# Optimization experiments

Hardware: AMD Instinct MI355X
Metric: run time of the kernel (lower is better)

The kernel has to match this reference:

```python
import jax, jax.numpy as jnp
import numpy as np

N, NFEAT, NHID1, NHID2 = 16384, 128, 128, 64

def setup_inputs() -> dict:
    key = jax.random.key(0)
    k1, k2, k3, k4 = jax.random.split(key, 4)
    feature = jax.random.normal(k1, (N, NFEAT), dtype=jnp.float32)
    # dense (row-normalized) adjacency surrogate
    adj = jax.random.uniform(k2, (N, N), dtype=jnp.float32) / N
    W1 = jax.random.normal(k3, (NFEAT, NHID1), dtype=jnp.float32) / np.sqrt(NFEAT)
    b1 = jnp.zeros((NHID1,), dtype=jnp.float32)
    W2 = jax.random.normal(k4, (NHID1, NHID2), dtype=jnp.float32) / np.sqrt(NHID1)
    b2 = jnp.zeros((NHID2,), dtype=jnp.float32)
    return {"feature": feature, "adj": adj, "W1": W1, "b1": b1, "W2": W2, "b2": b2}

def reference(feature, adj, W1, b1, W2, b2):
    # layer 1: support = X@W1; agg = A@support; relu
    h = jax.nn.relu(adj @ (feature @ W1) + b1)
    # dropout is identity in eval mode
    # layer 2
    out = adj @ (h @ W2) + b2
    return out
```

## Files before the change

### kernel.cpp

```cpp
#include <hip/hip_runtime.h>
#include <stdint.h>

typedef float  f32x4  __attribute__((ext_vector_type(4)));
typedef short  short8 __attribute__((ext_vector_type(8)));
typedef __bf16 bf16x8 __attribute__((ext_vector_type(8)));

__device__ __forceinline__ unsigned short f2bf(float f) {
    unsigned u = __builtin_bit_cast(unsigned, f);
    unsigned r = u + 0x7fffu + ((u >> 16) & 1u);
    return (unsigned short)(r >> 16);
}

__device__ __forceinline__ short8 cvt8(f32x4 a, f32x4 b) {
    short8 r;
    r[0] = (short)f2bf(a[0]); r[1] = (short)f2bf(a[1]);
    r[2] = (short)f2bf(a[2]); r[3] = (short)f2bf(a[3]);
    r[4] = (short)f2bf(b[0]); r[5] = (short)f2bf(b[1]);
    r[6] = (short)f2bf(b[2]); r[7] = (short)f2bf(b[3]);
    return r;
}

typedef const __attribute__((address_space(1))) void* gas_p;
typedef __attribute__((address_space(3))) void*       las_p;
__device__ __forceinline__ void gld_lds16(const void* g, void* l) {
    __builtin_amdgcn_global_load_lds((gas_p)g, (las_p)l, 16, 0, 0);
}

__device__ __forceinline__ f32x4 mfma16(short8 a, short8 b, f32x4 c) {
    return __builtin_amdgcn_mfma_f32_16x16x32_bf16(
        __builtin_bit_cast(bf16x8, a), __builtin_bit_cast(bf16x8, b), c, 0, 0, 0);
}

template<int NMAT>
__global__ __launch_bounds__(256) void k_xw_t(const float* __restrict__ X,
                                              const float* __restrict__ W,
                                              short* __restrict__ St, int M) {
    constexpr int K   = 128;
    constexpr int NPT = NMAT / 4;
    __shared__ float Xs[64][129];
    __shared__ float Ws[K][NMAT];

    const int tid = threadIdx.x;
    const int m0  = blockIdx.x * 64;

    constexpr int WCH = K * NMAT / 4 / 256;
    #pragma unroll
    for (int j = 0; j < WCH; ++j) {
        int ch = tid + j * 256;
        ((float4*)Ws)[ch] = ((const float4*)W)[ch];
    }
    #pragma unroll
    for (int j = 0; j < 8; ++j) {
        int ch = tid + j * 256;
        int r = ch >> 5, c4 = ch & 31;
        float4 v = *(const float4*)(X + (size_t)(m0 + r) * K + c4 * 4);
        Xs[r][c4 * 4 + 0] = v.x; Xs[r][c4 * 4 + 1] = v.y;
        Xs[r][c4 * 4 + 2] = v.z; Xs[r][c4 * 4 + 3] = v.w;
    }
    __syncthreads();

    const int m  = tid & 63;
    const int n0 = (tid >> 6) * NPT;
    float acc[NPT];
    #pragma unroll
    for (int i = 0; i < NPT; ++i) acc[i] = 0.f;

    for (int k = 0; k < K; ++k) {
        float x = Xs[m][k];
        #pragma unroll
        for (int i = 0; i < NPT; i += 4) {
            float4 w = *(const float4*)&Ws[k][n0 + i];
            acc[i + 0] += x * w.x; acc[i + 1] += x * w.y;
            acc[i + 2] += x * w.z; acc[i + 3] += x * w.w;
        }
    }
    #pragma unroll
    for (int i = 0; i < NPT; ++i)
        St[(size_t)(n0 + i) * M + m0 + m] = (short)f2bf(acc[i]);
}

template<int BN, bool RELU>
__global__ __launch_bounds__(256, 1) void k_adj_gemm(const float* __restrict__ A,
                                                     const short* __restrict__ Bt,
                                                     const float* __restrict__ bias,
                                                     float* __restrict__ out,
                                                     int M, int K) {
    constexpr int BM   = 64, BK = 64;
    constexpr int NF   = BN / 16;
    constexpr int BCH  = BN * BK * 2 / (256 * 16);
    constexpr int VMH  = BCH + 16;
    constexpr int VML  = BCH;

    __shared__ short Bs[4][BN * 64];

    const int tid  = threadIdx.x;
    const int wave = tid >> 6, lane = tid & 63;
    const int lr   = lane & 15, lk = lane >> 4;
    const int row0 = blockIdx.x * BM;
    const int row_g = row0 + wave * 16 + lr;

    const char* Abase = (const char*)A + (size_t)row_g * K * 4 + lk * 32;

    const int key   = (lr & 7) << 4;
    const int offs0 = (lk * 16) ^ key;
    const int offs1 = (64 + lk * 16) ^ key;

    f32x4 acc[NF];
    #pragma unroll
    for (int n = 0; n < NF; ++n) acc[n] = (f32x4)0.f;

    f32x4 bA0[16], bA1[16];
    const int NT  = K / BK;
    const int NTM = NT - 1;

#define LOAD_SLOT(QARR, BI, TT)                                                 \
    {                                                                           \
        const char* p = Abase + (size_t)(TT) * 256;                             \
        QARR[(BI) + 0] = *(const f32x4*)(p);                                    \
        QARR[(BI) + 1] = *(const f32x4*)(p + 16);                               \
        QARR[(BI) + 2] = *(const f32x4*)(p + 128);                              \
        QARR[(BI) + 3] = *(const f32x4*)(p + 144);                              \
    }
#define LOAD_BATCH(QARR, T0)                                                    \
    {                                                                           \
        LOAD_SLOT(QARR, 0,  ((T0) + 0) & NTM)                                   \
        LOAD_SLOT(QARR, 4,  ((T0) + 1) & NTM)                                   \
        LOAD_SLOT(QARR, 8,  ((T0) + 2) & NTM)                                   \
        LOAD_SLOT(QARR, 12, ((T0) + 3) & NTM)                                   \
    }
#define STAGE_B(BUF, KTP)                                                       \
    {                                                                           \
        _Pragma("unroll")                                                       \
        for (int j = 0; j < BCH; ++j) {                                         \
            int o = (tid + j * 256) * 16;          \
            int r = o >> 7, w = o & 127;                                        \
            const char* src = (const char*)Bt + (size_t)r * (K * 2)             \
                              + (size_t)(KTP) * 128 + (w ^ ((r & 7) << 4));     \
            gld_lds16(src, (char*)&Bs[BUF][0] + o);                             \
        }                                                                       \
    }

    LOAD_BATCH(bA0, 0)
    STAGE_B(0, 0)
    LOAD_BATCH(bA1, 4)

#define ITER(KT, QARR, J4, CB, NB, VM, BATCH_STMT)                              \
    {                                                                           \
                        \
        short8 fa0 = cvt8(QARR[(J4) + 0], QARR[(J4) + 1]);                      \
        short8 fa1 = cvt8(QARR[(J4) + 2], QARR[(J4) + 3]);                      \
        { int ktn = ((KT) + 1) & NTM; STAGE_B(NB, ktn) }                        \
        BATCH_STMT                                                              \
        __builtin_amdgcn_sched_barrier(0);                                      \
            \
        asm volatile("s_waitcnt vmcnt(%0)" :: "i"(VM) : "memory");              \
        __builtin_amdgcn_s_barrier();                     \
        __builtin_amdgcn_sched_barrier(0);                                      \
        _Pragma("unroll")                                                       \
        for (int n = 0; n < NF; ++n) {                                          \
            short8 b0 = *(const short8*)((const char*)&Bs[CB][0]                \
                                         + n * 2048 + lr * 128 + offs0);        \
            acc[n] = mfma16(fa0, b0, acc[n]);                                   \
            short8 b1 = *(const short8*)((const char*)&Bs[CB][0]                \
                                         + n * 2048 + lr * 128 + offs1);        \
            acc[n] = mfma16(fa1, b1, acc[n]);                                   \
        }                                                                       \
    }

    for (int g = 0; g < 32; ++g) {
        int t = g * 8;
        ITER(t + 0, bA0, 0,  0, 1, VMH, )
        ITER(t + 1, bA0, 4,  1, 2, VML, )
        ITER(t + 2, bA0, 8,  2, 3, VML, )
        ITER(t + 3, bA0, 12, 3, 0, VMH, LOAD_BATCH(bA0, (t + 3) + 5))
        ITER(t + 4, bA1, 0,  0, 1, VMH, )
        ITER(t + 5, bA1, 4,  1, 2, VML, )
        ITER(t + 6, bA1, 8,  2, 3, VML, )
        ITER(t + 7, bA1, 12, 3, 0, VMH, LOAD_BATCH(bA1, (t + 7) + 5))
    }
#undef ITER
#undef LOAD_BATCH
#undef LOAD_SLOT
#undef STAGE_B

    #pragma unroll
    for (int n = 0; n < NF; ++n) {
        int col = n * 16 + lr;
        float bv = bias[col];
        #pragma unroll
        for (int j = 0; j < 4; ++j) {
            int row = row0 + wave * 16 + lk * 4 + j;
            float v = acc[n][j] + bv;
            if (RELU) v = fmaxf(v, 0.f);
            out[(size_t)row * BN + col] = v;
        }
    }
}

extern "C" void kernel_launch(void* const* d_in, const int* in_sizes, int n_in,
                              void* d_out, int out_size, void* d_ws, size_t ws_size,
                              hipStream_t stream) {
    const int N = 16384, NH1 = 128, NH2 = 64;
    const float* feature = (const float*)d_in[0];
    const float* adj     = (const float*)d_in[1];
    const float* W1      = (const float*)d_in[2];
    const float* b1      = (const float*)d_in[3];
    const float* W2      = (const float*)d_in[4];
    const float* b2      = (const float*)d_in[5];

    short* S1t = (short*)d_ws;
    float* h   = (float*)((char*)d_ws + (4u << 20));
    short* S2t = (short*)((char*)d_ws + (12u << 20));

    k_xw_t<NH1><<<N / 64, 256, 0, stream>>>(feature, W1, S1t, N);
    k_adj_gemm<NH1, true ><<<N / 64, 256, 0, stream>>>(adj, S1t, b1, h, N, N);
    k_xw_t<NH2><<<N / 64, 256, 0, stream>>>(h, W2, S2t, N);
    k_adj_gemm<NH2, false><<<N / 64, 256, 0, stream>>>(adj, S2t, b2, (float*)d_out, N, N);
    (void)in_sizes; (void)n_in; (void)out_size; (void)ws_size;
}
```

Measured before the change: 486.8 us.

## Stage B tiles in bursts of four with eight LDS buffers

Replaces the per-iteration single-tile B staging (4 LDS buffers) with a burst that stages four B tiles plus the next A register batch at once into an 8-buffer LDS ring, with graded vmcnt waits per iteration. The aim is to issue memory loads in larger groups and keep more tiles in flight, hiding global latency in the adjacency GEMM. It doubles LDS use for B and changes the wait accounting, which could reduce occupancy or introduce stalls if the vmcnt thresholds are off.

```diff
diff --git a/kernel.cpp b/kernel.cpp
--- a/kernel.cpp
+++ b/kernel.cpp
@@ -88,10 +88,12 @@
     constexpr int BM   = 64, BK = 64;
     constexpr int NF   = BN / 16;
     constexpr int BCH  = BN * BK * 2 / (256 * 16);
-    constexpr int VMH  = BCH + 16;
-    constexpr int VML  = BCH;
-
-    __shared__ short Bs[4][BN * 64];
+    constexpr int VM0  = 7 * BCH + 32;
+    constexpr int VM1  = 6 * BCH + 32;
+    constexpr int VM2  = 5 * BCH + 32;
+    constexpr int VM3  = 4 * BCH + 32;
+
+    __shared__ short Bs[8][BN * 64];
 
     const int tid  = threadIdx.x;
     const int wave = tid >> 6, lane = tid & 63;
@@ -128,31 +130,34 @@
         LOAD_SLOT(QARR, 8,  ((T0) + 2) & NTM)                                   \
         LOAD_SLOT(QARR, 12, ((T0) + 3) & NTM)                                   \
     }
-#define STAGE_B(BUF, KTP)                                                       \
+#define STAGE_B1(BUF, KTP)                                                      \
     {                                                                           \
         _Pragma("unroll")                                                       \
         for (int j = 0; j < BCH; ++j) {                                         \
             int o = (tid + j * 256) * 16;          \
             int r = o >> 7, w = o & 127;                                        \
             const char* src = (const char*)Bt + (size_t)r * (K * 2)             \
-                              + (size_t)(KTP) * 128 + (w ^ ((r & 7) << 4));     \
+                              + (size_t)((KTP) & NTM) * 128 + (w ^ ((r & 7) << 4)); \
             gld_lds16(src, (char*)&Bs[BUF][0] + o);                             \
         }                                                                       \
     }
-
-    LOAD_BATCH(bA0, 0)
-    STAGE_B(0, 0)
-    LOAD_BATCH(bA1, 4)
-
-#define ITER(KT, QARR, J4, CB, NB, VM, BATCH_STMT)                              \
-    {                                                                           \
-                        \
+#define STAGE_BURST(BF0, QARR, T0)                                              \
+    STAGE_B1((BF0) + 0, (T0) + 0)                                               \
+    STAGE_B1((BF0) + 1, (T0) + 1)                                               \
+    STAGE_B1((BF0) + 2, (T0) + 2)                                               \
+    STAGE_B1((BF0) + 3, (T0) + 3)                                               \
+    LOAD_BATCH(QARR, T0)
+
+    STAGE_BURST(0, bA1, 0)
+
+#define ITER(KT, QARR, J4, CB, VM, STAGE_STMT)                                  \
+    {                                                                           \
+                   \
         short8 fa0 = cvt8(QARR[(J4) + 0], QARR[(J4) + 1]);                      \
         short8 fa1 = cvt8(QARR[(J4) + 2], QARR[(J4) + 3]);                      \
-        { int ktn = ((KT) + 1) & NTM; STAGE_B(NB, ktn) }                        \
-        BATCH_STMT                                                              \
+        STAGE_STMT                                                              \
         __builtin_amdgcn_sched_barrier(0);                                      \
-            \
+                   \
         asm volatile("s_waitcnt vmcnt(%0)" :: "i"(VM) : "memory");              \
         __builtin_amdgcn_s_barrier();                     \
         __builtin_amdgcn_sched_barrier(0);                                      \
@@ -167,21 +172,22 @@
         }                                                                       \
     }
 
-    for (int g = 0; g < 32; ++g) {
-        int t = g * 8;
-        ITER(t + 0, bA0, 0,  0, 1, VMH, )
-        ITER(t + 1, bA0, 4,  1, 2, VML, )
-        ITER(t + 2, bA0, 8,  2, 3, VML, )
-        ITER(t + 3, bA0, 12, 3, 0, VMH, LOAD_BATCH(bA0, (t + 3) + 5))
-        ITER(t + 4, bA1, 0,  0, 1, VMH, )
-        ITER(t + 5, bA1, 4,  1, 2, VML, )
-        ITER(t + 6, bA1, 8,  2, 3, VML, )
-        ITER(t + 7, bA1, 12, 3, 0, VMH, LOAD_BATCH(bA1, (t + 7) + 5))
+    for (int d = 0; d < 32; ++d) {
+        int t = d * 8;
+        ITER(t + 0, bA1, 0,  0, VM0, STAGE_BURST(4, bA0, (t) + 4))
+        ITER(t + 1, bA1, 4,  1, VM1, )
+        ITER(t + 2, bA1, 8,  2, VM2, )
+        ITER(t + 3, bA1, 12, 3, VM3, )
+        ITER(t + 4, bA0, 0,  4, VM0, STAGE_BURST(0, bA1, (t) + 8))
+        ITER(t + 5, bA0, 4,  5, VM1, )
+        ITER(t + 6, bA0, 8,  6, VM2, )
+        ITER(t + 7, bA0, 12, 7, VM3, )
     }
 #undef ITER
+#undef STAGE_BURST
+#undef STAGE_B1
 #undef LOAD_BATCH
 #undef LOAD_SLOT
-#undef STAGE_B
 
     #pragma unroll
     for (int n = 0; n < NF; ++n) {
```

After: 489.7 us. About the same (+0.6%).

## Write bf16 adjacency during first aggregation and reuse it in second GEMM

Applied to the files above, without the earlier changes.

The first adjacency GEMM now also stores its bf16-converted A fragments to a 512 MB workspace buffer, laid out in fragment order. The second GEMM reads those pre-converted fragments instead of re-reading the fp32 adjacency, which halves its A traffic and removes its conversion work. The cost is 512 MB of extra writes in the first kernel plus more workspace, and the vmcnt waits are adjusted to account for the added stores.

```diff
diff --git a/kernel.cpp b/kernel.cpp
--- a/kernel.cpp
+++ b/kernel.cpp
@@ -79,17 +79,17 @@
         St[(size_t)(n0 + i) * M + m0 + m] = (short)f2bf(acc[i]);
 }
 
-template<int BN, bool RELU>
-__global__ __launch_bounds__(256, 1) void k_adj_gemm(const float* __restrict__ A,
-                                                     const short* __restrict__ Bt,
-                                                     const float* __restrict__ bias,
-                                                     float* __restrict__ out,
-                                                     int M, int K) {
-    constexpr int BM   = 64, BK = 64;
-    constexpr int NF   = BN / 16;
-    constexpr int BCH  = BN * BK * 2 / (256 * 16);
-    constexpr int VMH  = BCH + 16;
-    constexpr int VML  = BCH;
+__global__ __launch_bounds__(256, 1) void k_adj_cvt(const float* __restrict__ A,
+                                                    const short* __restrict__ Bt,
+                                                    const float* __restrict__ bias,
+                                                    float* __restrict__ out,
+                                                    char* __restrict__ adj16,
+                                                    int M, int K) {
+    constexpr int BM  = 64, BK = 64, BN = 128;
+    constexpr int NF  = BN / 16;
+    constexpr int BCH = BN * BK * 2 / (256 * 16);
+    constexpr int VMH = BCH + 18;
+    constexpr int VML = BCH + 2;
 
     __shared__ short Bs[4][BN * 64];
 
@@ -100,6 +100,7 @@
     const int row_g = row0 + wave * 16 + lr;
 
     const char* Abase = (const char*)A + (size_t)row_g * K * 4 + lk * 32;
+    char* Cbase = adj16 + (size_t)blockIdx.x * 256 * 8192 + tid * 32;
 
     const int key   = (lr & 7) << 4;
     const int offs0 = (lk * 16) ^ key;
@@ -132,10 +133,10 @@
     {                                                                           \
         _Pragma("unroll")                                                       \
         for (int j = 0; j < BCH; ++j) {                                         \
-            int o = (tid + j * 256) * 16;          \
+            int o = (tid + j * 256) * 16;                                       \
             int r = o >> 7, w = o & 127;                                        \
             const char* src = (const char*)Bt + (size_t)r * (K * 2)             \
-                              + (size_t)(KTP) * 128 + (w ^ ((r & 7) << 4));     \
+                              + (size_t)((KTP) & NTM) * 128 + (w ^ ((r & 7) << 4)); \
             gld_lds16(src, (char*)&Bs[BUF][0] + o);                             \
         }                                                                       \
     }
@@ -146,15 +147,13 @@
 
 #define ITER(KT, QARR, J4, CB, NB, VM, BATCH_STMT)                              \
     {                                                                           \
-                        \
         short8 fa0 = cvt8(QARR[(J4) + 0], QARR[(J4) + 1]);                      \
         short8 fa1 = cvt8(QARR[(J4) + 2], QARR[(J4) + 3]);                      \
         { int ktn = ((KT) + 1) & NTM; STAGE_B(NB, ktn) }                        \
         BATCH_STMT                                                              \
         __builtin_amdgcn_sched_barrier(0);                                      \
-            \
         asm volatile("s_waitcnt vmcnt(%0)" :: "i"(VM) : "memory");              \
-        __builtin_amdgcn_s_barrier();                     \
+        __builtin_amdgcn_s_barrier();                                           \
         __builtin_amdgcn_sched_barrier(0);                                      \
         _Pragma("unroll")                                                       \
         for (int n = 0; n < NF; ++n) {                                          \
@@ -165,6 +164,9 @@
                                          + n * 2048 + lr * 128 + offs1);        \
             acc[n] = mfma16(fa1, b1, acc[n]);                                   \
         }                                                                       \
+        __builtin_amdgcn_sched_barrier(0);                                      \
+        { char* dst = Cbase + (size_t)(KT) * 8192;                              \
+          *(short8*)(dst) = fa0; *(short8*)(dst + 16) = fa1; }                  \
     }
 
     for (int g = 0; g < 32; ++g) {
@@ -179,9 +181,9 @@
         ITER(t + 7, bA1, 12, 3, 0, VMH, LOAD_BATCH(bA1, (t + 7) + 5))
     }
 #undef ITER
+#undef STAGE_B
 #undef LOAD_BATCH
 #undef LOAD_SLOT
-#undef STAGE_B
 
     #pragma unroll
     for (int n = 0; n < NF; ++n) {
@@ -190,9 +192,117 @@
         #pragma unroll
         for (int j = 0; j < 4; ++j) {
             int row = row0 + wave * 16 + lk * 4 + j;
-            float v = acc[n][j] + bv;
-            if (RELU) v = fmaxf(v, 0.f);
-            out[(size_t)row * BN + col] = v;
+            out[(size_t)row * BN + col] = fmaxf(acc[n][j] + bv, 0.f);
+        }
+    }
+}
+
+__global__ __launch_bounds__(256, 1) void k_adj_pre(const char* __restrict__ adj16,
+                                                    const short* __restrict__ Bt,
+                                                    const float* __restrict__ bias,
+                                                    float* __restrict__ out,
+                                                    int M, int K) {
+    constexpr int BM  = 64, BK = 64, BN = 64;
+    constexpr int NF  = BN / 16;
+    constexpr int BCH = BN * BK * 2 / (256 * 16);
+    constexpr int VMH = BCH + 8;
+    constexpr int VML = BCH;
+
+    __shared__ short Bs[4][BN * 64];
+
+    const int tid  = threadIdx.x;
+    const int wave = tid >> 6, lane = tid & 63;
+    const int lr   = lane & 15, lk = lane >> 4;
+    const int row0 = blockIdx.x * BM;
+
+    const char* Cbase = adj16 + (size_t)blockIdx.x * 256 * 8192 + tid * 32;
+
+    const int key   = (lr & 7) << 4;
+    const int offs0 = (lk * 16) ^ key;
+    const int offs1 = (64 + lk * 16) ^ key;
+
+    f32x4 acc[NF];
+    #pragma unroll
+    for (int n = 0; n < NF; ++n) acc[n] = (f32x4)0.f;
+
+    uint4 bA0[8], bA1[8];
+    const int NT  = K / BK;
+    const int NTM = NT - 1;
+
+#define LOAD_SLOT(QARR, BI, TT)                                                 \
+    {                                                                           \
+        const char* p = Cbase + (size_t)(TT) * 8192;                            \
+        QARR[(BI) + 0] = *(const uint4*)(p);                                    \
+        QARR[(BI) + 1] = *(const uint4*)(p + 16);                               \
+    }
+#define LOAD_BATCH(QARR, T0)                                                    \
+    {                                                                           \
+        LOAD_SLOT(QARR, 0, ((T0) + 0) & NTM)                                    \
+        LOAD_SLOT(QARR, 2, ((T0) + 1) & NTM)                                    \
+        LOAD_SLOT(QARR, 4, ((T0) + 2) & NTM)                                    \
+        LOAD_SLOT(QARR, 6, ((T0) + 3) & NTM)                                    \
+    }
+#define STAGE_B(BUF, KTP)                                                       \
+    {                                                                           \
+        _Pragma("unroll")                                                       \
+        for (int j = 0; j < BCH; ++j) {                                         \
+            int o = (tid + j * 256) * 16;                                       \
+            int r = o >> 7, w = o & 127;                                        \
+            const char* src = (const char*)Bt + (size_t)r * (K * 2)             \
+                              + (size_t)((KTP) & NTM) * 128 + (w ^ ((r & 7) << 4)); \
+            gld_lds16(src, (char*)&Bs[BUF][0] + o);                             \
+        }                                                                       \
+    }
+
+    LOAD_BATCH(bA0, 0)
+    STAGE_B(0, 0)
+    LOAD_BATCH(bA1, 4)
+
+#define ITER(KT, QARR, J4, CB, NB, VM, BATCH_STMT)                              \
+    {                                                                           \
+        short8 fa0 = __builtin_bit_cast(short8, QARR[(J4) + 0]);                \
+        short8 fa1 = __builtin_bit_cast(short8, QARR[(J4) + 1]);                \
+        { int ktn = ((KT) + 1) & NTM; STAGE_B(NB, ktn) }                        \
+        BATCH_STMT                                                              \
+        __builtin_amdgcn_sched_barrier(0);                                      \
+        asm volatile("s_waitcnt vmcnt(%0)" :: "i"(VM) : "memory");              \
+        __builtin_amdgcn_s_barrier();                                           \
+        __builtin_amdgcn_sched_barrier(0);                                      \
+        _Pragma("unroll")                                                       \
+        for (int n = 0; n < NF; ++n) {                                          \
+            short8 b0 = *(const short8*)((const char*)&Bs[CB][0]                \
+                                         + n * 2048 + lr * 128 + offs0);        \
+            acc[n] = mfma16(fa0, b0, acc[n]);                                   \
+            short8 b1 = *(const short8*)((const char*)&Bs[CB][0]                \
+                                         + n * 2048 + lr * 128 + offs1);        \
+            acc[n] = mfma16(fa1, b1, acc[n]);                                   \
+        }                                                                       \
+    }
+
+    for (int g = 0; g < 32; ++g) {
+        int t = g * 8;
+        ITER(t + 0, bA0, 0, 0, 1, VMH, )
+        ITER(t + 1, bA0, 2, 1, 2, VML, )
+        ITER(t + 2, bA0, 4, 2, 3, VML, )
+        ITER(t + 3, bA0, 6, 3, 0, VMH, LOAD_BATCH(bA0, (t + 3) + 5))
+        ITER(t + 4, bA1, 0, 0, 1, VMH, )
+        ITER(t + 5, bA1, 2, 1, 2, VML, )
+        ITER(t + 6, bA1, 4, 2, 3, VML, )
+        ITER(t + 7, bA1, 6, 3, 0, VMH, LOAD_BATCH(bA1, (t + 7) + 5))
+    }
+#undef ITER
+#undef STAGE_B
+#undef LOAD_BATCH
+#undef LOAD_SLOT
+
+    #pragma unroll
+    for (int n = 0; n < NF; ++n) {
+        int col = n * 16 + lr;
+        float bv = bias[col];
+        #pragma unroll
+        for (int j = 0; j < 4; ++j) {
+            int row = row0 + wave * 16 + lk * 4 + j;
+            out[(size_t)row * BN + col] = acc[n][j] + bv;
         }
     }
 }
@@ -208,13 +318,14 @@
     const float* W2      = (const float*)d_in[4];
     const float* b2      = (const float*)d_in[5];
 
-    short* S1t = (short*)d_ws;
-    float* h   = (float*)((char*)d_ws + (4u << 20));
-    short* S2t = (short*)((char*)d_ws + (12u << 20));
+    short* S1t  = (short*)d_ws;
+    float* h    = (float*)((char*)d_ws + (4u << 20));
+    short* S2t  = (short*)((char*)d_ws + (12u << 20));
+    char*  a16  = (char*)d_ws + (16u << 20);
 
     k_xw_t<NH1><<<N / 64, 256, 0, stream>>>(feature, W1, S1t, N);
-    k_adj_gemm<NH1, true ><<<N / 64, 256, 0, stream>>>(adj, S1t, b1, h, N, N);
+    k_adj_cvt <<<N / 64, 256, 0, stream>>>(adj, S1t, b1, h, a16, N, N);
     k_xw_t<NH2><<<N / 64, 256, 0, stream>>>(h, W2, S2t, N);
-    k_adj_gemm<NH2, false><<<N / 64, 256, 0, stream>>>(adj, S2t, b2, (float*)d_out, N, N);
+    k_adj_pre <<<N / 64, 256, 0, stream>>>(a16, S2t, b2, (float*)d_out, N, N);
     (void)in_sizes; (void)n_in; (void)out_size; (void)ws_size;
 }
```

Result: slower. 607.5 us (+24.8%).
